# Kernel tuning notes

Hardware: AMD Instinct MI355X
Metric: run time of the kernel (lower is better)

Reference implementation:

```python
import jax, jax.numpy as jnp
import numpy as np

EMBED_DIM = 1024
NUM_HEADS = 16
HEAD_DIM = EMBED_DIM // NUM_HEADS


def setup_inputs() -> dict:
    key = jax.random.key(0)
    k_x, k_wqkv, k_bqkv, k_wo, k_bo = jax.random.split(key, 5)
    bound = 1.0 / np.sqrt(EMBED_DIM)
    x = jax.random.normal(k_x, (2, 2048, EMBED_DIM), dtype=jnp.float32)
    # torch Linear weight is [out, in]; store as [in, out] for x @ W
    W_qkv = jax.random.uniform(k_wqkv, (EMBED_DIM, 3 * EMBED_DIM), minval=-bound, maxval=bound, dtype=jnp.float32)
    b_qkv = jax.random.uniform(k_bqkv, (3 * EMBED_DIM,), minval=-bound, maxval=bound, dtype=jnp.float32)
    W_out = jax.random.uniform(k_wo, (EMBED_DIM, EMBED_DIM), minval=-bound, maxval=bound, dtype=jnp.float32)
    b_out = jax.random.uniform(k_bo, (EMBED_DIM,), minval=-bound, maxval=bound, dtype=jnp.float32)
    return {"x": x, "W_qkv": W_qkv, "b_qkv": b_qkv, "W_out": W_out, "b_out": b_out}


def reference(x, W_qkv, b_qkv, W_out, b_out):
    B, T, D = x.shape
    H, Hd = NUM_HEADS, HEAD_DIM
    qkv = x @ W_qkv + b_qkv                      # [B,T,3D]
    qkv = qkv.reshape(B, T, 3, H, Hd)
    q = qkv[:, :, 0].transpose(0, 2, 1, 3)       # [B,H,T,Hd]
    k = qkv[:, :, 1].transpose(0, 2, 1, 3)
    v = qkv[:, :, 2].transpose(0, 2, 1, 3)
    scores = jnp.einsum('bhqd,bhkd->bhqk', q, k) / jnp.sqrt(jnp.float32(Hd))
    attn = jax.nn.softmax(scores, axis=-1)       # [B,H,T,T]
    out = jnp.einsum('bhqk,bhkd->bhqd', attn, v) # [B,H,T,Hd]
    out = out.transpose(0, 2, 1, 3).reshape(B, T, D)
    return out @ W_out + b_out
```

## Files before the change

### kernel.cpp

```cpp
#include <hip/hip_runtime.h>
#include <hip/hip_bf16.h>

#define B_   2
#define T_   2048
#define D_   1024
#define H_   16
#define HD_  64
#define M_TOT (B_*T_)
#define N_QKV (3*D_)

typedef __attribute__((ext_vector_type(8))) short bf16x8;
typedef __attribute__((ext_vector_type(4))) float f32x4;
typedef __attribute__((ext_vector_type(16))) float f32x16;

static __device__ __forceinline__ short f2bf(float f) {
    union { __hip_bfloat16 h; short s; } u;
    u.h = __float2bfloat16(f);
    return u.s;
}
static __device__ __forceinline__ unsigned pack2(float a, float b) {
    return (unsigned)(unsigned short)f2bf(a) | ((unsigned)(unsigned short)f2bf(b) << 16);
}
static __device__ __forceinline__ unsigned cvtpk(float lo, float hi) {
    unsigned r;
    asm("v_cvt_pk_bf16_f32 %0, %1, %2" : "=v"(r) : "v"(lo), "v"(hi));
    return r;
}
static __device__ __forceinline__ float exp2_fast(float x) {
    return __builtin_amdgcn_exp2f(x);
}
static __device__ __forceinline__ f32x16 zero16() {
    f32x16 z;
    #pragma unroll
    for (int i = 0; i < 16; ++i) z[i] = 0.f;
    return z;
}
static __device__ __forceinline__ void gload16(const void* g, void* l) {
    __builtin_amdgcn_global_load_lds(
        (__attribute__((address_space(1))) unsigned int*)(unsigned long long)g,
        (__attribute__((address_space(3))) unsigned int*)l, 16, 0, 0);
}

__global__ __launch_bounds__(256) void convert_x(const float* __restrict__ x,
                                                 short* __restrict__ xb, int n8) {
    int i = blockIdx.x * blockDim.x + threadIdx.x;
    if (i >= n8) return;
    const float4* p = (const float4*)x + (size_t)i * 2;
    float4 a = p[0], b = p[1];
    bf16x8 o;
    o[0]=f2bf(a.x); o[1]=f2bf(a.y); o[2]=f2bf(a.z); o[3]=f2bf(a.w);
    o[4]=f2bf(b.x); o[5]=f2bf(b.y); o[6]=f2bf(b.z); o[7]=f2bf(b.w);
    *((bf16x8*)xb + i) = o;
}

__global__ __launch_bounds__(256) void transpose_convert(const float* __restrict__ in,
                                                         short* __restrict__ out,
                                                         int K, int N) {
    __shared__ short tile[64][65];
    int k0 = blockIdx.y * 64, n0 = blockIdx.x * 64;
    int t = threadIdx.x;
    #pragma unroll
    for (int i = 0; i < 16; ++i) {
        int idx = i * 256 + t;
        int r = idx >> 6, c = idx & 63;
        tile[r][c] = f2bf(in[(size_t)(k0 + r) * N + n0 + c]);
    }
    __syncthreads();
    #pragma unroll
    for (int i = 0; i < 16; ++i) {
        int idx = i * 256 + t;
        int r = idx >> 6, c = idx & 63;
        out[(size_t)(n0 + r) * K + k0 + c] = tile[c][r];
    }
}

#define QSC 0.18033688f
template<int BM, int BN, int MODE>
__global__ __launch_bounds__(256)
void gemm_dl(const short* __restrict__ A, const short* __restrict__ BT,
             const float* __restrict__ bias, int M, int N, int K,
             short* __restrict__ qo, short* __restrict__ ko,
             short* __restrict__ vo, float* __restrict__ fo) {
    constexpr int BUF = (BM + BN) * 64;
    constexpr int NL = (BM + BN) / 64;
    __shared__ char smem[3 * BUF];
    const int t = threadIdx.x, w = t >> 6, l = t & 63;
    const int qi_l = l & 15, hi_l = l >> 4;
    const int m0 = blockIdx.y * BM, n0 = blockIdx.x * BN;
    const int wr = w >> 1, wc = w & 1;
    constexpr int MI = BM / 32, NI = BN / 32;

    f32x4 acc[MI][NI];
    #pragma unroll
    for (int mi = 0; mi < MI; ++mi)
        #pragma unroll
        for (int ni = 0; ni < NI; ++ni)
            acc[mi][ni] = (f32x4){0.f, 0.f, 0.f, 0.f};

    const int lrow = l >> 2;
    const int lch  = ((l & 3) ^ (lrow & 3)) * 8;

    auto stage = [&](char* dst, int k0) {
        #pragma unroll
        for (int i = 0; i < BM / 64; ++i) {
            int rb = w * (BM / 4) + i * 16;
            gload16(A + (size_t)(m0 + rb + lrow) * K + k0 + lch, dst + rb * 64);
        }
        #pragma unroll
        for (int i = 0; i < BN / 64; ++i) {
            int rb = w * (BN / 4) + i * 16;
            gload16(BT + (size_t)(n0 + rb + lrow) * K + k0 + lch, dst + BM * 64 + rb * 64);
        }
    };

    const int nt = K / 32;
    stage(smem, 0);
    if (nt > 1) stage(smem + BUF, 32);
    for (int it = 0; it < nt; ++it) {
        if (it + 2 < nt) {
            stage(smem + ((it + 2) % 3) * BUF, (it + 2) * 32);
            if constexpr (NL == 4)      asm volatile("s_waitcnt vmcnt(8)" ::: "memory");
            else if constexpr (NL == 3) asm volatile("s_waitcnt vmcnt(6)" ::: "memory");
            else                        asm volatile("s_waitcnt vmcnt(0)" ::: "memory");
        } else if (it + 1 < nt) {
            if constexpr (NL == 4)      asm volatile("s_waitcnt vmcnt(4)" ::: "memory");
            else if constexpr (NL == 3) asm volatile("s_waitcnt vmcnt(3)" ::: "memory");
            else                        asm volatile("s_waitcnt vmcnt(0)" ::: "memory");
        } else {
            asm volatile("s_waitcnt vmcnt(0)" ::: "memory");
        }
        __builtin_amdgcn_s_barrier();

        char* sA = smem + (it % 3) * BUF;
        char* sB = sA + BM * 64;
        bf16x8 af[MI], bfr[NI];
        #pragma unroll
        for (int mi = 0; mi < MI; ++mi) {
            int row = wr * (BM / 2) + mi * 16 + qi_l;
            int ad = row * 64 + ((hi_l ^ (row & 3)) * 16);
            af[mi] = *(const bf16x8*)(sA + ad);
        }
        #pragma unroll
        for (int ni = 0; ni < NI; ++ni) {
            int row = wc * (BN / 2) + ni * 16 + qi_l;
            int ad = row * 64 + ((hi_l ^ (row & 3)) * 16);
            bfr[ni] = *(const bf16x8*)(sB + ad);
        }
        #pragma unroll
        for (int mi = 0; mi < MI; ++mi)
            #pragma unroll
            for (int ni = 0; ni < NI; ++ni)
                acc[mi][ni] = __builtin_amdgcn_mfma_f32_16x16x32_bf16(af[mi], bfr[ni], acc[mi][ni], 0, 0, 0);

        __builtin_amdgcn_s_barrier();
    }

    #pragma unroll
    for (int mi = 0; mi < MI; ++mi) {
        int rbase = m0 + wr * (BM / 2) + mi * 16 + 4 * hi_l;
        #pragma unroll
        for (int ni = 0; ni < NI; ++ni) {
            int n = n0 + wc * (BN / 2) + ni * 16 + qi_l;
            float bv = bias[n];
            #pragma unroll
            for (int r = 0; r < 4; ++r) {
                int mm = rbase + r;
                float c = acc[mi][ni][r] + bv;
                if (MODE == 0) {
                    int which = n >> 10, rest = n & 1023;
                    int h = rest >> 6, d = rest & 63;
                    int b = mm >> 11, tq = mm & 2047;
                    size_t bh = (size_t)(b * H_ + h);
                    if (which == 0)      qo[(bh * T_ + tq) * HD_ + d] = f2bf(c * QSC);
                    else if (which == 1) ko[(bh * T_ + tq) * HD_ + d] = f2bf(c);
                    else                 vo[(bh * HD_ + d) * T_ + tq] = f2bf(c);
                } else {
                    fo[(size_t)mm * N + n] = c;
                }
            }
        }
    }
}

__global__ __launch_bounds__(512)
void attn(const short* __restrict__ q, const short* __restrict__ k,
          const short* __restrict__ vt, short* __restrict__ ao) {
    __shared__ char smem[32768];

    const int t = threadIdx.x, w = t >> 6, l = t & 63;
    const int q32 = l & 31, hi2 = l >> 5;
    const int swz = (l & 7) << 4;
    const int bh = blockIdx.x;
    const int q0 = blockIdx.y * 256 + w * 32;

    const short* qptr = q + ((size_t)bh * T_ + q0) * HD_;
    const short* kbase = k + (size_t)bh * T_ * HD_;
    const short* vbase = vt + (size_t)bh * HD_ * T_;

    const int srow = w * 8 + (l >> 3);
    const int sch  = ((l & 7) ^ (l >> 3)) * 8;

    bf16x8 qa[4];
    #pragma unroll
    for (int kc = 0; kc < 4; ++kc)
        qa[kc] = *(const bf16x8*)(qptr + q32 * HD_ + kc * 16 + hi2 * 8);

    f32x16 o0 = zero16(), o1 = zero16();
    float m = -1e30f, lsum = 0.f;

    gload16(kbase + (size_t)srow * HD_ + sch, smem + srow * 128);
    gload16(vbase + (size_t)srow * T_ + sch,  smem + 8192 + srow * 128);
    __syncthreads();

    int cur = 0;
    for (int kb = 0; kb < T_; kb += 64) {
        char* sK = smem + cur * 16384;
        char* sV = sK + 8192;
        if (kb + 64 < T_) {
            char* nK = smem + (cur ^ 1) * 16384;
            gload16(kbase + (size_t)(kb + 64 + srow) * HD_ + sch, nK + srow * 128);
            gload16(vbase + (size_t)srow * T_ + (kb + 64) + sch,  nK + 8192 + srow * 128);
        }

        f32x16 s0 = zero16(), s1 = zero16();
        #pragma unroll
        for (int kc = 0; kc < 4; ++kc) {
            int off = (kc * 32 + hi2 * 16) ^ swz;
            bf16x8 kf0 = *(const bf16x8*)(sK + q32 * 128 + off);
            s0 = __builtin_amdgcn_mfma_f32_32x32x16_bf16(kf0, qa[kc], s0, 0, 0, 0);
            bf16x8 kf1 = *(const bf16x8*)(sK + (32 + q32) * 128 + off);
            s1 = __builtin_amdgcn_mfma_f32_32x32x16_bf16(kf1, qa[kc], s1, 0, 0, 0);
        }

        float a8[8];
        #pragma unroll
        for (int i = 0; i < 8; ++i)
            a8[i] = fmaxf(fmaxf(s0[i], s0[i + 8]), fmaxf(s1[i], s1[i + 8]));
        float b4_0 = fmaxf(a8[0], a8[1]), b4_1 = fmaxf(a8[2], a8[3]);
        float b4_2 = fmaxf(a8[4], a8[5]), b4_3 = fmaxf(a8[6], a8[7]);
        float tm = fmaxf(fmaxf(b4_0, b4_1), fmaxf(b4_2, b4_3));
        tm = fmaxf(tm, __shfl_xor(tm, 32));

        if (!__all(tm <= m + 8.f)) {
            float mnew = fmaxf(m, tm);
            float fsc = exp2_fast(m - mnew);
            lsum *= fsc;
            #pragma unroll
            for (int i = 0; i < 16; ++i) { o0[i] *= fsc; o1[i] *= fsc; }
            m = mnew;
        }

        #pragma unroll
        for (int i = 0; i < 16; ++i) {
            s0[i] = exp2_fast(s0[i] - m);
            s1[i] = exp2_fast(s1[i] - m);
        }
        float p8[8];
        #pragma unroll
        for (int i = 0; i < 8; ++i)
            p8[i] = (s0[i] + s0[i + 8]) + (s1[i] + s1[i + 8]);
        float psum = ((p8[0] + p8[1]) + (p8[2] + p8[3])) + ((p8[4] + p8[5]) + (p8[6] + p8[7]));
        psum += __shfl_xor(psum, 32);
        lsum += psum;

        unsigned pk0[8], pk1[8];
        #pragma unroll
        for (int p = 0; p < 8; ++p) {
            pk0[p] = cvtpk(s0[2 * p], s0[2 * p + 1]);
            pk1[p] = cvtpk(s1[2 * p], s1[2 * p + 1]);
        }

        #pragma unroll
        for (int c = 0; c < 4; ++c) {
            unsigned w0 = (c & 2) ? pk1[(c & 1) * 4 + 0] : pk0[(c & 1) * 4 + 0];
            unsigned w1 = (c & 2) ? pk1[(c & 1) * 4 + 1] : pk0[(c & 1) * 4 + 1];
            unsigned w2 = (c & 2) ? pk1[(c & 1) * 4 + 2] : pk0[(c & 1) * 4 + 2];
            unsigned w3 = (c & 2) ? pk1[(c & 1) * 4 + 3] : pk0[(c & 1) * 4 + 3];
            unsigned t0 = hi2 ? w0 : w2;
            unsigned t1 = hi2 ? w1 : w3;
            unsigned r0 = __shfl_xor(t0, 32);
            unsigned r1 = __shfl_xor(t1, 32);
            union { unsigned u[4]; bf16x8 v; } uf;
            uf.u[0] = hi2 ? r0 : w0;
            uf.u[1] = hi2 ? r1 : w1;
            uf.u[2] = hi2 ? w2 : r0;
            uf.u[3] = hi2 ? w3 : r1;
            bf16x8 pf = uf.v;

            int off = (c * 32 + hi2 * 16) ^ swz;
            bf16x8 vf0 = *(const bf16x8*)(sV + q32 * 128 + off);
            o0 = __builtin_amdgcn_mfma_f32_32x32x16_bf16(vf0, pf, o0, 0, 0, 0);
            bf16x8 vf1 = *(const bf16x8*)(sV + (32 + q32) * 128 + off);
            o1 = __builtin_amdgcn_mfma_f32_32x32x16_bf16(vf1, pf, o1, 0, 0, 0);
        }

        __syncthreads();
        cur ^= 1;
    }

    const float inv = 1.f / lsum;
    const int b = bh >> 4, h = bh & 15;
    const int tq = q0 + q32;
    unsigned* aou = (unsigned*)(ao + ((size_t)(b * T_ + tq)) * D_ + h * HD_);
    #pragma unroll
    for (int pr = 0; pr < 8; ++pr) {
        int d0 = 2 * (pr & 1) + 8 * (pr >> 1) + 4 * hi2;
        aou[d0 >> 1]        = pack2(o0[2 * pr] * inv, o0[2 * pr + 1] * inv);
        aou[(32 + d0) >> 1] = pack2(o1[2 * pr] * inv, o1[2 * pr + 1] * inv);
    }
}

extern "C" void kernel_launch(void* const* d_in, const int* in_sizes, int n_in,
                              void* d_out, int out_size, void* d_ws, size_t ws_size,
                              hipStream_t stream) {
    const float* x    = (const float*)d_in[0];
    const float* Wqkv = (const float*)d_in[1];
    const float* bqkv = (const float*)d_in[2];
    const float* Wout = (const float*)d_in[3];
    const float* bout = (const float*)d_in[4];
    float* out = (float*)d_out;

    char* ws = (char*)d_ws;
    short* xb  = (short*)(ws);
    short* WqT = (short*)(ws + ((size_t)8  << 20));
    short* WoT = (short*)(ws + ((size_t)14 << 20));
    short* qb  = (short*)(ws + ((size_t)16 << 20));
    short* kb  = (short*)(ws + ((size_t)24 << 20));
    short* vtb = (short*)(ws + ((size_t)32 << 20));
    short* aob = (short*)(ws + ((size_t)40 << 20));

    convert_x<<<(M_TOT * D_ / 8 + 255) / 256, 256, 0, stream>>>(x, xb, M_TOT * D_ / 8);
    transpose_convert<<<dim3(N_QKV / 64, D_ / 64), 256, 0, stream>>>(Wqkv, WqT, D_, N_QKV);
    transpose_convert<<<dim3(D_ / 64, D_ / 64), 256, 0, stream>>>(Wout, WoT, D_, D_);

    gemm_dl<128, 128, 0><<<dim3(N_QKV / 128, M_TOT / 128), 256, 0, stream>>>(
        xb, WqT, bqkv, M_TOT, N_QKV, D_, qb, kb, vtb, nullptr);

    attn<<<dim3(B_ * H_, T_ / 256), 512, 0, stream>>>(qb, kb, vtb, aob);

    gemm_dl<128, 64, 1><<<dim3(D_ / 64, M_TOT / 128), 256, 0, stream>>>(
        aob, WoT, bout, M_TOT, D_, D_, nullptr, nullptr, nullptr, out);
}
```

Measured before the change: 125.5 us.

## Process two 32-row query tiles per wave in attention to reuse K/V fragments

Each attention wave now handles 64 query rows (two 32-row tiles, A and B) instead of 32, and the block shrinks from 8 to 4 waves while covering the same 256 queries. K and V fragments read from LDS are reused across both query tiles, which halves LDS reads per MFMA and interleaves independent MFMA chains. Staging of K/V tiles is spread over fewer threads, with two loads each. The cost is roughly double the accumulator and score register footprint, which may lower occupancy or cause spills. The output conversion also moves from pack2 to cvtpk.

```diff
diff --git a/kernel.cpp b/kernel.cpp
--- a/kernel.cpp
+++ b/kernel.cpp
@@ -182,7 +182,7 @@
     }
 }
 
-__global__ __launch_bounds__(512)
+__global__ __launch_bounds__(256)
 void attn(const short* __restrict__ q, const short* __restrict__ k,
           const short* __restrict__ vt, short* __restrict__ ao) {
     __shared__ char smem[32768];
@@ -191,122 +191,195 @@
     const int q32 = l & 31, hi2 = l >> 5;
     const int swz = (l & 7) << 4;
     const int bh = blockIdx.x;
-    const int q0 = blockIdx.y * 256 + w * 32;
-
-    const short* qptr = q + ((size_t)bh * T_ + q0) * HD_;
+    const int qbase = blockIdx.y * 256 + w * 64;
+
+    const short* qptrA = q + ((size_t)bh * T_ + qbase) * HD_;
+    const short* qptrB = qptrA + 32 * HD_;
     const short* kbase = k + (size_t)bh * T_ * HD_;
     const short* vbase = vt + (size_t)bh * HD_ * T_;
 
-    const int srow = w * 8 + (l >> 3);
+    const int srow = w * 16 + (l >> 3);
     const int sch  = ((l & 7) ^ (l >> 3)) * 8;
 
-    bf16x8 qa[4];
-    #pragma unroll
-    for (int kc = 0; kc < 4; ++kc)
-        qa[kc] = *(const bf16x8*)(qptr + q32 * HD_ + kc * 16 + hi2 * 8);
-
-    f32x16 o0 = zero16(), o1 = zero16();
-    float m = -1e30f, lsum = 0.f;
-
-    gload16(kbase + (size_t)srow * HD_ + sch, smem + srow * 128);
-    gload16(vbase + (size_t)srow * T_ + sch,  smem + 8192 + srow * 128);
+    bf16x8 qaA[4], qaB[4];
+    #pragma unroll
+    for (int kc = 0; kc < 4; ++kc) {
+        qaA[kc] = *(const bf16x8*)(qptrA + q32 * HD_ + kc * 16 + hi2 * 8);
+        qaB[kc] = *(const bf16x8*)(qptrB + q32 * HD_ + kc * 16 + hi2 * 8);
+    }
+
+    f32x16 oA0 = zero16(), oA1 = zero16(), oB0 = zero16(), oB1 = zero16();
+    float mA = -1e30f, lA = 0.f, mB = -1e30f, lB = 0.f;
+
+    auto stage = [&](int kb, char* dst) {
+        gload16(kbase + (size_t)(kb + srow) * HD_ + sch,     dst + srow * 128);
+        gload16(kbase + (size_t)(kb + srow + 8) * HD_ + sch, dst + (srow + 8) * 128);
+        gload16(vbase + (size_t)srow * T_ + kb + sch,        dst + 8192 + srow * 128);
+        gload16(vbase + (size_t)(srow + 8) * T_ + kb + sch,  dst + 8192 + (srow + 8) * 128);
+    };
+
+    stage(0, smem);
     __syncthreads();
 
     int cur = 0;
     for (int kb = 0; kb < T_; kb += 64) {
         char* sK = smem + cur * 16384;
         char* sV = sK + 8192;
-        if (kb + 64 < T_) {
-            char* nK = smem + (cur ^ 1) * 16384;
-            gload16(kbase + (size_t)(kb + 64 + srow) * HD_ + sch, nK + srow * 128);
-            gload16(vbase + (size_t)srow * T_ + (kb + 64) + sch,  nK + 8192 + srow * 128);
-        }
-
-        f32x16 s0 = zero16(), s1 = zero16();
+        if (kb + 64 < T_) stage(kb + 64, smem + (cur ^ 1) * 16384);
+
+        f32x16 sA0 = zero16(), sA1 = zero16(), sB0 = zero16(), sB1 = zero16();
         #pragma unroll
         for (int kc = 0; kc < 4; ++kc) {
             int off = (kc * 32 + hi2 * 16) ^ swz;
             bf16x8 kf0 = *(const bf16x8*)(sK + q32 * 128 + off);
-            s0 = __builtin_amdgcn_mfma_f32_32x32x16_bf16(kf0, qa[kc], s0, 0, 0, 0);
             bf16x8 kf1 = *(const bf16x8*)(sK + (32 + q32) * 128 + off);
-            s1 = __builtin_amdgcn_mfma_f32_32x32x16_bf16(kf1, qa[kc], s1, 0, 0, 0);
-        }
-
-        float a8[8];
-        #pragma unroll
-        for (int i = 0; i < 8; ++i)
-            a8[i] = fmaxf(fmaxf(s0[i], s0[i + 8]), fmaxf(s1[i], s1[i + 8]));
-        float b4_0 = fmaxf(a8[0], a8[1]), b4_1 = fmaxf(a8[2], a8[3]);
-        float b4_2 = fmaxf(a8[4], a8[5]), b4_3 = fmaxf(a8[6], a8[7]);
-        float tm = fmaxf(fmaxf(b4_0, b4_1), fmaxf(b4_2, b4_3));
-        tm = fmaxf(tm, __shfl_xor(tm, 32));
-
-        if (!__all(tm <= m + 8.f)) {
-            float mnew = fmaxf(m, tm);
-            float fsc = exp2_fast(m - mnew);
-            lsum *= fsc;
-            #pragma unroll
-            for (int i = 0; i < 16; ++i) { o0[i] *= fsc; o1[i] *= fsc; }
-            m = mnew;
-        }
-
-        #pragma unroll
-        for (int i = 0; i < 16; ++i) {
-            s0[i] = exp2_fast(s0[i] - m);
-            s1[i] = exp2_fast(s1[i] - m);
-        }
-        float p8[8];
-        #pragma unroll
-        for (int i = 0; i < 8; ++i)
-            p8[i] = (s0[i] + s0[i + 8]) + (s1[i] + s1[i + 8]);
-        float psum = ((p8[0] + p8[1]) + (p8[2] + p8[3])) + ((p8[4] + p8[5]) + (p8[6] + p8[7]));
-        psum += __shfl_xor(psum, 32);
-        lsum += psum;
-
-        unsigned pk0[8], pk1[8];
-        #pragma unroll
-        for (int p = 0; p < 8; ++p) {
-            pk0[p] = cvtpk(s0[2 * p], s0[2 * p + 1]);
-            pk1[p] = cvtpk(s1[2 * p], s1[2 * p + 1]);
+            sA0 = __builtin_amdgcn_mfma_f32_32x32x16_bf16(kf0, qaA[kc], sA0, 0, 0, 0);
+            sA1 = __builtin_amdgcn_mfma_f32_32x32x16_bf16(kf1, qaA[kc], sA1, 0, 0, 0);
+            sB0 = __builtin_amdgcn_mfma_f32_32x32x16_bf16(kf0, qaB[kc], sB0, 0, 0, 0);
+            sB1 = __builtin_amdgcn_mfma_f32_32x32x16_bf16(kf1, qaB[kc], sB1, 0, 0, 0);
+        }
+
+        unsigned pkA0[8], pkA1[8];
+        {
+            float a8[8];
+            #pragma unroll
+            for (int i = 0; i < 8; ++i)
+                a8[i] = fmaxf(fmaxf(sA0[i], sA0[i + 8]), fmaxf(sA1[i], sA1[i + 8]));
+            float b0 = fmaxf(a8[0], a8[1]), b1 = fmaxf(a8[2], a8[3]);
+            float b2 = fmaxf(a8[4], a8[5]), b3 = fmaxf(a8[6], a8[7]);
+            float tm = fmaxf(fmaxf(b0, b1), fmaxf(b2, b3));
+            tm = fmaxf(tm, __shfl_xor(tm, 32));
+            if (!__all(tm <= mA + 8.f)) {
+                float mnew = fmaxf(mA, tm);
+                float fsc = exp2_fast(mA - mnew);
+                lA *= fsc;
+                #pragma unroll
+                for (int i = 0; i < 16; ++i) { oA0[i] *= fsc; oA1[i] *= fsc; }
+                mA = mnew;
+            }
+            #pragma unroll
+            for (int i = 0; i < 16; ++i) {
+                sA0[i] = exp2_fast(sA0[i] - mA);
+                sA1[i] = exp2_fast(sA1[i] - mA);
+            }
+            float p8[8];
+            #pragma unroll
+            for (int i = 0; i < 8; ++i)
+                p8[i] = (sA0[i] + sA0[i + 8]) + (sA1[i] + sA1[i + 8]);
+            float ps = ((p8[0] + p8[1]) + (p8[2] + p8[3])) + ((p8[4] + p8[5]) + (p8[6] + p8[7]));
+            ps += __shfl_xor(ps, 32);
+            lA += ps;
+            #pragma unroll
+            for (int p = 0; p < 8; ++p) {
+                pkA0[p] = cvtpk(sA0[2 * p], sA0[2 * p + 1]);
+                pkA1[p] = cvtpk(sA1[2 * p], sA1[2 * p + 1]);
+            }
+        }
+        unsigned pkB0[8], pkB1[8];
+        {
+            float a8[8];
+            #pragma unroll
+            for (int i = 0; i < 8; ++i)
+                a8[i] = fmaxf(fmaxf(sB0[i], sB0[i + 8]), fmaxf(sB1[i], sB1[i + 8]));
+            float b0 = fmaxf(a8[0], a8[1]), b1 = fmaxf(a8[2], a8[3]);
+            float b2 = fmaxf(a8[4], a8[5]), b3 = fmaxf(a8[6], a8[7]);
+            float tm = fmaxf(fmaxf(b0, b1), fmaxf(b2, b3));
+            tm = fmaxf(tm, __shfl_xor(tm, 32));
+            if (!__all(tm <= mB + 8.f)) {
+                float mnew = fmaxf(mB, tm);
+                float fsc = exp2_fast(mB - mnew);
+                lB *= fsc;
+                #pragma unroll
+                for (int i = 0; i < 16; ++i) { oB0[i] *= fsc; oB1[i] *= fsc; }
+                mB = mnew;
+            }
+            #pragma unroll
+            for (int i = 0; i < 16; ++i) {
+                sB0[i] = exp2_fast(sB0[i] - mB);
+                sB1[i] = exp2_fast(sB1[i] - mB);
+            }
+            float p8[8];
+            #pragma unroll
+            for (int i = 0; i < 8; ++i)
+                p8[i] = (sB0[i] + sB0[i + 8]) + (sB1[i] + sB1[i + 8]);
+            float ps = ((p8[0] + p8[1]) + (p8[2] + p8[3])) + ((p8[4] + p8[5]) + (p8[6] + p8[7]));
+            ps += __shfl_xor(ps, 32);
+            lB += ps;
+            #pragma unroll
+            for (int p = 0; p < 8; ++p) {
+                pkB0[p] = cvtpk(sB0[2 * p], sB0[2 * p + 1]);
+                pkB1[p] = cvtpk(sB1[2 * p], sB1[2 * p + 1]);
+            }
         }
 
         #pragma unroll
         for (int c = 0; c < 4; ++c) {
-            unsigned w0 = (c & 2) ? pk1[(c & 1) * 4 + 0] : pk0[(c & 1) * 4 + 0];
-            unsigned w1 = (c & 2) ? pk1[(c & 1) * 4 + 1] : pk0[(c & 1) * 4 + 1];
-            unsigned w2 = (c & 2) ? pk1[(c & 1) * 4 + 2] : pk0[(c & 1) * 4 + 2];
-            unsigned w3 = (c & 2) ? pk1[(c & 1) * 4 + 3] : pk0[(c & 1) * 4 + 3];
-            unsigned t0 = hi2 ? w0 : w2;
-            unsigned t1 = hi2 ? w1 : w3;
-            unsigned r0 = __shfl_xor(t0, 32);
-            unsigned r1 = __shfl_xor(t1, 32);
-            union { unsigned u[4]; bf16x8 v; } uf;
-            uf.u[0] = hi2 ? r0 : w0;
-            uf.u[1] = hi2 ? r1 : w1;
-            uf.u[2] = hi2 ? w2 : r0;
-            uf.u[3] = hi2 ? w3 : r1;
-            bf16x8 pf = uf.v;
-
             int off = (c * 32 + hi2 * 16) ^ swz;
             bf16x8 vf0 = *(const bf16x8*)(sV + q32 * 128 + off);
-            o0 = __builtin_amdgcn_mfma_f32_32x32x16_bf16(vf0, pf, o0, 0, 0, 0);
             bf16x8 vf1 = *(const bf16x8*)(sV + (32 + q32) * 128 + off);
-            o1 = __builtin_amdgcn_mfma_f32_32x32x16_bf16(vf1, pf, o1, 0, 0, 0);
+
+            {
+                unsigned w0 = (c & 2) ? pkA1[(c & 1) * 4 + 0] : pkA0[(c & 1) * 4 + 0];
+                unsigned w1 = (c & 2) ? pkA1[(c & 1) * 4 + 1] : pkA0[(c & 1) * 4 + 1];
+                unsigned w2 = (c & 2) ? pkA1[(c & 1) * 4 + 2] : pkA0[(c & 1) * 4 + 2];
+                unsigned w3 = (c & 2) ? pkA1[(c & 1) * 4 + 3] : pkA0[(c & 1) * 4 + 3];
+                unsigned t0 = hi2 ? w0 : w2;
+                unsigned t1 = hi2 ? w1 : w3;
+                unsigned r0 = __shfl_xor(t0, 32);
+                unsigned r1 = __shfl_xor(t1, 32);
+                union { unsigned u[4]; bf16x8 v; } uf;
+                uf.u[0] = hi2 ? r0 : w0;
+                uf.u[1] = hi2 ? r1 : w1;
+                uf.u[2] = hi2 ? w2 : r0;
+                uf.u[3] = hi2 ? w3 : r1;
+                oA0 = __builtin_amdgcn_mfma_f32_32x32x16_bf16(vf0, uf.v, oA0, 0, 0, 0);
+                oA1 = __builtin_amdgcn_mfma_f32_32x32x16_bf16(vf1, uf.v, oA1, 0, 0, 0);
+            }
+            {
+                unsigned w0 = (c & 2) ? pkB1[(c & 1) * 4 + 0] : pkB0[(c & 1) * 4 + 0];
+                unsigned w1 = (c & 2) ? pkB1[(c & 1) * 4 + 1] : pkB0[(c & 1) * 4 + 1];
+                unsigned w2 = (c & 2) ? pkB1[(c & 1) * 4 + 2] : pkB0[(c & 1) * 4 + 2];
+                unsigned w3 = (c & 2) ? pkB1[(c & 1) * 4 + 3] : pkB0[(c & 1) * 4 + 3];
+                unsigned t0 = hi2 ? w0 : w2;
+                unsigned t1 = hi2 ? w1 : w3;
+                unsigned r0 = __shfl_xor(t0, 32);
+                unsigned r1 = __shfl_xor(t1, 32);
+                union { unsigned u[4]; bf16x8 v; } uf;
+                uf.u[0] = hi2 ? r0 : w0;
+                uf.u[1] = hi2 ? r1 : w1;
+                uf.u[2] = hi2 ? w2 : r0;
+                uf.u[3] = hi2 ? w3 : r1;
+                oB0 = __builtin_amdgcn_mfma_f32_32x32x16_bf16(vf0, uf.v, oB0, 0, 0, 0);
+                oB1 = __builtin_amdgcn_mfma_f32_32x32x16_bf16(vf1, uf.v, oB1, 0, 0, 0);
+            }
         }
 
         __syncthreads();
         cur ^= 1;
     }
 
-    const float inv = 1.f / lsum;
     const int b = bh >> 4, h = bh & 15;
-    const int tq = q0 + q32;
-    unsigned* aou = (unsigned*)(ao + ((size_t)(b * T_ + tq)) * D_ + h * HD_);
-    #pragma unroll
-    for (int pr = 0; pr < 8; ++pr) {
-        int d0 = 2 * (pr & 1) + 8 * (pr >> 1) + 4 * hi2;
-        aou[d0 >> 1]        = pack2(o0[2 * pr] * inv, o0[2 * pr + 1] * inv);
-        aou[(32 + d0) >> 1] = pack2(o1[2 * pr] * inv, o1[2 * pr + 1] * inv);
+    {
+        const float inv = 1.f / lA;
+        const int tq = qbase + q32;
+        unsigned* aou = (unsigned*)(ao + ((size_t)(b * T_ + tq)) * D_ + h * HD_);
+        #pragma unroll
+        for (int pr = 0; pr < 8; ++pr) {
+            int d0 = 2 * (pr & 1) + 8 * (pr >> 1) + 4 * hi2;
+            aou[d0 >> 1]        = cvtpk(oA0[2 * pr] * inv, oA0[2 * pr + 1] * inv);
+            aou[(32 + d0) >> 1] = cvtpk(oA1[2 * pr] * inv, oA1[2 * pr + 1] * inv);
+        }
+    }
+    {
+        const float inv = 1.f / lB;
+        const int tq = qbase + 32 + q32;
+        unsigned* aou = (unsigned*)(ao + ((size_t)(b * T_ + tq)) * D_ + h * HD_);
+        #pragma unroll
+        for (int pr = 0; pr < 8; ++pr) {
+            int d0 = 2 * (pr & 1) + 8 * (pr >> 1) + 4 * hi2;
+            aou[d0 >> 1]        = cvtpk(oB0[2 * pr] * inv, oB0[2 * pr + 1] * inv);
+            aou[(32 + d0) >> 1] = cvtpk(oB1[2 * pr] * inv, oB1[2 * pr + 1] * inv);
+        }
     }
 }
 
@@ -336,7 +409,7 @@
     gemm_dl<128, 128, 0><<<dim3(N_QKV / 128, M_TOT / 128), 256, 0, stream>>>(
         xb, WqT, bqkv, M_TOT, N_QKV, D_, qb, kb, vtb, nullptr);
 
-    attn<<<dim3(B_ * H_, T_ / 256), 512, 0, stream>>>(qb, kb, vtb, aob);
+    attn<<<dim3(B_ * H_, T_ / 256), 256, 0, stream>>>(qb, kb, vtb, aob);
 
     gemm_dl<128, 64, 1><<<dim3(D_ / 64, M_TOT / 128), 256, 0, stream>>>(
         aob, WoT, bout, M_TOT, D_, D_, nullptr, nullptr, nullptr, out);
```

Result: slower. 140.7 us (+12.1%).
